# Kernel optimization log

Measured on AMD Instinct MI355X. Metric: run time of the kernel, lower is better.

The kernel has to match this reference:

```python
import jax, jax.numpy as jnp
import numpy as np

N_NODES = 100000
N_EDGES = 1600000
IN_FEATS = 128
HIDDEN = 128
OUT_DIM = 128


def setup_inputs() -> dict:
    key = jax.random.key(0)
    ks = jax.random.split(key, 8)
    x = jax.random.normal(ks[0], (N_NODES, IN_FEATS), dtype=jnp.float32)
    W1 = jax.random.normal(ks[1], (IN_FEATS, HIDDEN), dtype=jnp.float32) * (1.0 / np.sqrt(IN_FEATS))
    b1 = jnp.zeros((HIDDEN,), dtype=jnp.float32)
    W2 = jax.random.normal(ks[2], (HIDDEN, HIDDEN), dtype=jnp.float32) * (1.0 / np.sqrt(HIDDEN))
    b2 = jnp.zeros((HIDDEN,), dtype=jnp.float32)
    W3 = jax.random.normal(ks[3], (HIDDEN, OUT_DIM), dtype=jnp.float32) * (1.0 / np.sqrt(HIDDEN))
    b3 = jnp.zeros((OUT_DIM,), dtype=jnp.float32)
    edge_src = jax.random.randint(ks[4], (N_EDGES,), 0, N_NODES, dtype=jnp.int32)
    edge_dst = jax.random.randint(ks[5], (N_EDGES,), 0, N_NODES, dtype=jnp.int32)
    return {"x": x, "W1": W1, "b1": b1, "W2": W2, "b2": b2, "W3": W3, "b3": b3,
            "edge_src": edge_src, "edge_dst": edge_dst}


def _mean_agg(h, edge_src, edge_dst, inv_deg):
    # gather src features, scatter-sum to dst, divide by in-degree (mean)
    summed = jax.ops.segment_sum(h[edge_src], edge_dst, num_segments=N_NODES)
    return summed * inv_deg[:, None]


def reference(x, W1, b1, W2, b2, W3, b3, edge_src, edge_dst):
    # in-degree (clamped to 1 to avoid div-by-zero, matching mean over empty = 0)
    deg = jax.ops.segment_sum(jnp.ones((N_EDGES,), dtype=jnp.float32), edge_dst,
                              num_segments=N_NODES)
    inv_deg = 1.0 / jnp.maximum(deg, 1.0)

    # DGL GINConv (eps=0, mean): h = Linear(h + mean_neighbors(h))
    h = x
    h = (h + _mean_agg(h, edge_src, edge_dst, inv_deg)) @ W1 + b1
    h = jax.nn.relu(h)  # dropout inactive in eval mode
    h = (h + _mean_agg(h, edge_src, edge_dst, inv_deg)) @ W2 + b2
    h = jax.nn.relu(h)
    h = (h + _mean_agg(h, edge_src, edge_dst, inv_deg)) @ W3 + b3
    return h
```

## Files before the change

kernel.cpp:

```cpp
#include <hip/hip_runtime.h>
#include <hip/hip_bf16.h>
#include <stdint.h>

#if __has_builtin(__builtin_amdgcn_cvt_pk_f32_fp8) && __has_builtin(__builtin_amdgcn_cvt_pk_fp8_f32)
#define FP8_HW 1
#else
#define FP8_HW 0
#include <hip/hip_fp8.h>
#endif

#define N_NODES 100000
#define N_EDGES 1600000
#define FEAT 128

#define BKT_SHIFT 8
#define BKT_SIZE  256
#define NB_BKT    391
#define BKT_CAP   5664
#define NB_SC     800
#define EPB_SC    2000

typedef uint16_t u16;
typedef uint32_t u32;
typedef __attribute__((ext_vector_type(8))) short bf16x8;
typedef __attribute__((ext_vector_type(4))) float f32x4;
typedef __attribute__((ext_vector_type(2))) float f32x2;

__device__ __forceinline__ u16 bf16_rn(float f){
  u32 u = __float_as_uint(f);
  u += 0x7FFFu + ((u >> 16) & 1u);
  return (u16)(u >> 16);
}
__device__ __forceinline__ float bf16_lo(u32 p){ return __uint_as_float(p << 16); }
__device__ __forceinline__ float bf16_hi(u32 p){ return __uint_as_float(p & 0xFFFF0000u); }

__device__ __forceinline__ void fp8x4_to_f32(u32 w, float* o){
#if FP8_HW
  f32x2 a = __builtin_amdgcn_cvt_pk_f32_fp8(w, false);
  f32x2 b = __builtin_amdgcn_cvt_pk_f32_fp8(w, true);
  o[0] = a.x; o[1] = a.y; o[2] = b.x; o[3] = b.y;
#else
  #pragma unroll
  for (int i = 0; i < 4; ++i){
    __hip_fp8_e4m3 t; t.__x = (uint8_t)((w >> (8 * i)) & 0xFF);
    o[i] = (float)t;
  }
#endif
}
__device__ __forceinline__ u32 f32x4_to_fp8(float a, float b, float c, float d){
#if FP8_HW
  u32 r = __builtin_amdgcn_cvt_pk_fp8_f32(a, b, 0, false);
  r = __builtin_amdgcn_cvt_pk_fp8_f32(c, d, r, true);
  return r;
#else
  __hip_fp8_e4m3 qa(a), qb(b), qc(c), qd(d);
  return (u32)qa.__x | ((u32)qb.__x << 8) | ((u32)qc.__x << 16) | ((u32)qd.__x << 24);
#endif
}

__device__ __forceinline__ void acc_row(uint2 r, f32x2* acc){
#if FP8_HW
  acc[0] += __builtin_amdgcn_cvt_pk_f32_fp8(r.x, false);
  acc[1] += __builtin_amdgcn_cvt_pk_f32_fp8(r.x, true);
  acc[2] += __builtin_amdgcn_cvt_pk_f32_fp8(r.y, false);
  acc[3] += __builtin_amdgcn_cvt_pk_f32_fp8(r.y, true);
#else
  float t0[4], t1[4];
  fp8x4_to_f32(r.x, t0); fp8x4_to_f32(r.y, t1);
  acc[0].x += t0[0]; acc[0].y += t0[1]; acc[1].x += t0[2]; acc[1].y += t0[3];
  acc[2].x += t1[0]; acc[2].y += t1[1]; acc[3].x += t1[2]; acc[3].y += t1[3];
#endif
}


__global__ __launch_bounds__(512) void hist_kernel(const int* __restrict__ dst,
                                                   int* __restrict__ hcnt){
  __shared__ int h[NB_BKT];
  for (int i = threadIdx.x; i < NB_BKT; i += 512) h[i] = 0;
  __syncthreads();
  int base = blockIdx.x * EPB_SC;
  for (int e = base + threadIdx.x; e < base + EPB_SC; e += 512)
    atomicAdd(&h[dst[e] >> BKT_SHIFT], 1);
  __syncthreads();
  for (int i = threadIdx.x; i < NB_BKT; i += 512)
    hcnt[blockIdx.x * NB_BKT + i] = h[i];
}

__global__ void hscan_kernel(int* __restrict__ hcnt, int* __restrict__ cursor){
  __shared__ int s[256];
  int b = blockIdx.x, t = threadIdx.x;
  int v[4]; int sum = 0;
  #pragma unroll
  for (int j = 0; j < 4; ++j){
    int blk = 4 * t + j;
    v[j] = (blk < NB_SC) ? hcnt[blk * NB_BKT + b] : 0;
    sum += v[j];
  }
  s[t] = sum;
  __syncthreads();
  for (int d = 1; d < 256; d <<= 1){
    int add = (t >= d) ? s[t - d] : 0;
    __syncthreads();
    s[t] += add;
    __syncthreads();
  }
  int excl = s[t] - sum;
  #pragma unroll
  for (int j = 0; j < 4; ++j){
    int blk = 4 * t + j;
    if (blk < NB_SC){ hcnt[blk * NB_BKT + b] = excl; excl += v[j]; }
  }
  if (t == 255) cursor[b] = s[255];
}

__global__ __launch_bounds__(512) void scatter_kernel(const int* __restrict__ src,
                                                      const int* __restrict__ dst,
                                                      const int* __restrict__ hcnt,
                                                      uint2* __restrict__ bbuf){
  __shared__ int cur[NB_BKT];
  for (int i = threadIdx.x; i < NB_BKT; i += 512)
    cur[i] = hcnt[blockIdx.x * NB_BKT + i];
  __syncthreads();
  int base = blockIdx.x * EPB_SC;
  for (int e = base + threadIdx.x; e < base + EPB_SC; e += 512){
    int d = dst[e];
    int b = d >> BKT_SHIFT;
    int p = atomicAdd(&cur[b], 1);
    bbuf[(size_t)b * BKT_CAP + p] = make_uint2((u32)src[e], (u32)(d & (BKT_SIZE - 1)));
  }
}

__global__ __launch_bounds__(1024) void csr_build_kernel(const uint2* __restrict__ bbuf,
                                 const int* __restrict__ cursor,
                                 int* __restrict__ offs, int* __restrict__ deg,
                                 float* __restrict__ inv_deg, int* __restrict__ eidx){
  __shared__ int hist[BKT_SIZE];
  __shared__ int s[BKT_SIZE];
  __shared__ int cu[BKT_SIZE];
  int b = blockIdx.x;
  int t = threadIdx.x;
  int lo = b * BKT_CAP;
  int hi = lo + cursor[b];
  if (t < BKT_SIZE) hist[t] = 0;
  __syncthreads();
  for (int e = lo + t; e < hi; e += 1024)
    atomicAdd(&hist[bbuf[e].y], 1);
  __syncthreads();
  int v = 0, pv = 0;
  if (t < BKT_SIZE){
    v  = hist[t];
    pv = (v + 7) & ~7;
    s[t] = pv;
  }
  __syncthreads();
  for (int d = 1; d < BKT_SIZE; d <<= 1){
    int add = (t < BKT_SIZE && t >= d) ? s[t - d] : 0;
    __syncthreads();
    if (t < BKT_SIZE && t >= d) s[t] += add;
    __syncthreads();
  }
  if (t < BKT_SIZE){
    int excl = s[t] - pv;
    int node = b * BKT_SIZE + t;
    if (node < N_NODES){
      offs[node]    = lo + excl;
      deg[node]     = v;
      inv_deg[node] = 1.0f / fmaxf((float)v, 1.0f);
      for (int p = v; p < pv; ++p) eidx[lo + excl + p] = 0;
    }
    s[t]  = excl;
    cu[t] = 0;
  }
  __syncthreads();
  for (int e = lo + t; e < hi; e += 1024){
    uint2 q = bbuf[e];
    int p = atomicAdd(&cu[q.y], 1);
    eidx[lo + s[q.y] + p] = (int)q.x;
  }
}


__global__ void cvt_x8_kernel(const float* __restrict__ x, uint2* __restrict__ X8){
  int i = blockIdx.x * 256 + threadIdx.x;
  const float4* p = (const float4*)x + (size_t)i * 2;
  float4 a = p[0], b = p[1];
  uint2 o;
  o.x = f32x4_to_fp8(a.x, a.y, a.z, a.w);
  o.y = f32x4_to_fp8(b.x, b.y, b.z, b.w);
  X8[i] = o;
}

__global__ void wprep3_kernel(const float* __restrict__ W1, const float* __restrict__ W2,
                              const float* __restrict__ W3, u16* __restrict__ Wp1,
                              u16* __restrict__ Wp2, u16* __restrict__ Wp3){
  int which = blockIdx.x >> 6;
  int b     = blockIdx.x & 63;
  const float* W = (which == 0) ? W1 : (which == 1) ? W2 : W3;
  u16*        Wp = (which == 0) ? Wp1 : (which == 1) ? Wp2 : Wp3;
  int idx = b * 256 + threadIdx.x;
  int j    = idx & 7;
  int lane = (idx >> 3) & 63;
  int t    = idx >> 9;
  int k0 = t & 3, n0 = t >> 2;
  int k = k0 * 32 + (lane >> 4) * 8 + j;
  int n = n0 * 16 + (lane & 15);
  Wp[idx] = bf16_rn(W[k * FEAT + n]);
}


template<int SM, int OUT>
__global__ __launch_bounds__(128, 8) void layer_kernel(
    const u32* __restrict__ n8,
    const u16* __restrict__ hb,
    const float* __restrict__ xf,
    const int* __restrict__ offs,
    const int* __restrict__ deg,
    const float* __restrict__ inv_deg,
    const int* __restrict__ eidx,
    const u16* __restrict__ Wp,
    const float* __restrict__ bias,
    u16* __restrict__ Hout,
    u32* __restrict__ H8out,
    float* __restrict__ Fout){
  __shared__ u16 Tt[16 * FEAT];
  const int tid   = threadIdx.x;
  const int wid   = tid >> 6;
  const int lane  = tid & 63;
  const int nsub  = lane >> 4;
  const int slice = lane & 15;
  const int base  = blockIdx.x * 16;
  const u32* gbase = n8 + slice * 2;

  for (int g = 0; g < 2; ++g){
    const int rrow = wid * 8 + (g << 2) + nsub;
    const int node = base + rrow;
    const int start = offs[node];
    const int cnt   = deg[node];
    const int pcnt  = (cnt + 7) & ~7;
    const int* ep = eidx + start;

    f32x2 acc[4];
    #pragma unroll
    for (int j = 0; j < 4; ++j) acc[j] = (f32x2){0.f, 0.f};

    uint2 rc[8];
    #pragma unroll
    for (int j = 0; j < 8; ++j) rc[j] = make_uint2(0u, 0u);
    if (pcnt > 0){
      uint4 q0 = *(const uint4*)ep;
      uint4 q1 = *(const uint4*)(ep + 4);
      rc[0] = *(const uint2*)(gbase + (size_t)q0.x * 32);
      rc[1] = *(const uint2*)(gbase + (size_t)q0.y * 32);
      rc[2] = *(const uint2*)(gbase + (size_t)q0.z * 32);
      rc[3] = *(const uint2*)(gbase + (size_t)q0.w * 32);
      rc[4] = *(const uint2*)(gbase + (size_t)q1.x * 32);
      rc[5] = *(const uint2*)(gbase + (size_t)q1.y * 32);
      rc[6] = *(const uint2*)(gbase + (size_t)q1.z * 32);
      rc[7] = *(const uint2*)(gbase + (size_t)q1.w * 32);
    }
    uint4 qn1 = *(const uint4*)(ep + 8);
    uint4 qn2 = *(const uint4*)(ep + 12);

    for (int e = 0; e < pcnt; e += 8){
      uint2 rn[8];
      rn[0] = *(const uint2*)(gbase + (size_t)qn1.x * 32);
      rn[1] = *(const uint2*)(gbase + (size_t)qn1.y * 32);
      rn[2] = *(const uint2*)(gbase + (size_t)qn1.z * 32);
      rn[3] = *(const uint2*)(gbase + (size_t)qn1.w * 32);
      rn[4] = *(const uint2*)(gbase + (size_t)qn2.x * 32);
      rn[5] = *(const uint2*)(gbase + (size_t)qn2.y * 32);
      rn[6] = *(const uint2*)(gbase + (size_t)qn2.z * 32);
      rn[7] = *(const uint2*)(gbase + (size_t)qn2.w * 32);
      qn1 = *(const uint4*)(ep + e + 16);
      qn2 = *(const uint4*)(ep + e + 20);
      #pragma unroll
      for (int j = 0; j < 8; ++j) acc_row(rc[j], acc);
      #pragma unroll
      for (int j = 0; j < 8; ++j) rc[j] = rn[j];
    }

    if (pcnt > cnt){
      float f = (float)(pcnt - cnt);
      uint2 rz = *(const uint2*)gbase;
      f32x2 z[4];
      #pragma unroll
      for (int j = 0; j < 4; ++j) z[j] = (f32x2){0.f, 0.f};
      acc_row(rz, z);
      #pragma unroll
      for (int j = 0; j < 4; ++j) acc[j] -= f * z[j];
    }

    const float w = inv_deg[node];
    float self[8];
    if (SM == 1){
      const float* sp = xf + (size_t)node * FEAT + slice * 8;
      float4 a = *(const float4*)sp;
      float4 b = *(const float4*)(sp + 4);
      self[0]=a.x; self[1]=a.y; self[2]=a.z; self[3]=a.w;
      self[4]=b.x; self[5]=b.y; self[6]=b.z; self[7]=b.w;
    } else {
      const u16* sp = hb + (size_t)node * FEAT + slice * 8;
      uint4 s0 = *(const uint4*)sp;
      self[0]=bf16_lo(s0.x); self[1]=bf16_hi(s0.x); self[2]=bf16_lo(s0.y); self[3]=bf16_hi(s0.y);
      self[4]=bf16_lo(s0.z); self[5]=bf16_hi(s0.z); self[6]=bf16_lo(s0.w); self[7]=bf16_hi(s0.w);
    }
    uint4 o;
    o.x = (u32)bf16_rn(self[0] + w*acc[0].x) | ((u32)bf16_rn(self[1] + w*acc[0].y) << 16);
    o.y = (u32)bf16_rn(self[2] + w*acc[1].x) | ((u32)bf16_rn(self[3] + w*acc[1].y) << 16);
    o.z = (u32)bf16_rn(self[4] + w*acc[2].x) | ((u32)bf16_rn(self[5] + w*acc[2].y) << 16);
    o.w = (u32)bf16_rn(self[6] + w*acc[3].x) | ((u32)bf16_rn(self[7] + w*acc[3].y) << 16);
    ((uint4*)Tt)[rrow * 16 + (slice ^ (rrow & 7))] = o;
  }
  __syncthreads();

  const int quad = lane >> 4;
  const int c    = lane & 15;

  bf16x8 A[4];
  #pragma unroll
  for (int k0 = 0; k0 < 4; ++k0){
    uint4 t = ((const uint4*)Tt)[c * 16 + ((quad + k0 * 4) ^ (c & 7))];
    A[k0] = *(const bf16x8*)&t;
  }
  if (OUT == 0) __syncthreads();

  f32x4 acc2[4];
  #pragma unroll
  for (int i = 0; i < 4; ++i) acc2[i] = (f32x4){0.f, 0.f, 0.f, 0.f};
  #pragma unroll
  for (int i = 0; i < 4; ++i){
    int n0 = wid * 4 + i;
    #pragma unroll
    for (int k0 = 0; k0 < 4; ++k0){
      bf16x8 b = *(const bf16x8*)(Wp + (size_t)(((n0 << 2) | k0) * 64 + lane) * 8);
      acc2[i] = __builtin_amdgcn_mfma_f32_16x16x32_bf16(A[k0], b, acc2[i], 0, 0, 0);
    }
  }
  #pragma unroll
  for (int i = 0; i < 4; ++i){
    int n0 = wid * 4 + i;
    float bv = bias[n0 * 16 + c];
    #pragma unroll
    for (int r = 0; r < 4; ++r){
      int rr  = quad * 4 + r;
      int col = n0 * 16 + c;
      if (OUT == 1){
        Fout[(size_t)(base + rr) * FEAT + col] = acc2[i][r] + bv;
      } else {
        float v = fmaxf(acc2[i][r] + bv, 0.f);
        Tt[rr * FEAT + (col ^ ((rr & 7) << 3))] = bf16_rn(v);
      }
    }
  }

  if (OUT == 0){
    __syncthreads();
    #pragma unroll
    for (int it = 0; it < 2; ++it){
      int p  = it * 128 + tid;
      int rr = p >> 4, qq = p & 15;
      int node = base + rr;
      uint4 d = ((const uint4*)Tt)[rr * 16 + (qq ^ (rr & 7))];
      *(uint4*)(Hout + (size_t)node * FEAT + qq * 8) = d;
      uint2 o8;
      o8.x = f32x4_to_fp8(bf16_lo(d.x), bf16_hi(d.x), bf16_lo(d.y), bf16_hi(d.y));
      o8.y = f32x4_to_fp8(bf16_lo(d.z), bf16_hi(d.z), bf16_lo(d.w), bf16_hi(d.w));
      *(uint2*)(H8out + (size_t)node * 32 + qq * 2) = o8;
    }
  }
}


static inline size_t align_up(size_t x){ return (x + 255) & ~(size_t)255; }

extern "C" void kernel_launch(void* const* d_in, const int* in_sizes, int n_in,
                              void* d_out, int out_size, void* d_ws, size_t ws_size,
                              hipStream_t stream){
  const float* x  = (const float*)d_in[0];
  const float* W1 = (const float*)d_in[1];
  const float* b1 = (const float*)d_in[2];
  const float* W2 = (const float*)d_in[3];
  const float* b2 = (const float*)d_in[4];
  const float* W3 = (const float*)d_in[5];
  const float* b3 = (const float*)d_in[6];
  const int* esrc = (const int*)d_in[7];
  const int* edst = (const int*)d_in[8];

  char* w = (char*)d_ws;
  int*   deg     = (int*)w;    w += align_up((size_t)N_NODES * 4);
  int*   offs    = (int*)w;    w += align_up((size_t)N_NODES * 4);
  float* inv_deg = (float*)w;  w += align_up((size_t)N_NODES * 4);
  int*   eidx    = (int*)w;    w += align_up((size_t)NB_BKT * BKT_CAP * 4);
  u16*   Wp1     = (u16*)w;    w += align_up((size_t)16384 * 2);
  u16*   Wp2     = (u16*)w;    w += align_up((size_t)16384 * 2);
  u16*   Wp3     = (u16*)w;    w += align_up((size_t)16384 * 2);
  u16*   Hb      = (u16*)w;    w += align_up((size_t)N_NODES * FEAT * 2);
  u32*   H8b     = (u32*)w;    w += align_up((size_t)N_NODES * 32 * 4);

  uint2* bbuf   = (uint2*)Hb;
  int*   cursor = (int*)H8b;
  int*   hcnt   = (int*)((char*)H8b + align_up((size_t)NB_BKT * 4));

  u16* Ha  = (u16*)d_out;
  u32* H8a = (u32*)((char*)d_out + (size_t)N_NODES * FEAT * 2);
  u32* X8  = (u32*)((char*)d_out + (size_t)N_NODES * FEAT * 3);

  hist_kernel<<<NB_SC, 512, 0, stream>>>(edst, hcnt);
  hscan_kernel<<<NB_BKT, 256, 0, stream>>>(hcnt, cursor);
  scatter_kernel<<<NB_SC, 512, 0, stream>>>(esrc, edst, hcnt, bbuf);
  csr_build_kernel<<<NB_BKT, 1024, 0, stream>>>(bbuf, cursor, offs, deg, inv_deg, eidx);

  wprep3_kernel<<<192, 256, 0, stream>>>(W1, W2, W3, Wp1, Wp2, Wp3);
  cvt_x8_kernel<<<N_EDGES / 256, 256, 0, stream>>>(x, (uint2*)X8);

  const int LAYER_BLOCKS = N_NODES / 16;

  layer_kernel<1, 0><<<LAYER_BLOCKS, 128, 0, stream>>>(
      X8, (const u16*)nullptr, x, offs, deg, inv_deg, eidx, Wp1, b1,
      Ha, H8a, (float*)nullptr);

  layer_kernel<0, 0><<<LAYER_BLOCKS, 128, 0, stream>>>(
      H8a, Ha, (const float*)nullptr, offs, deg, inv_deg, eidx, Wp2, b2,
      Hb, H8b, (float*)nullptr);

  layer_kernel<0, 1><<<LAYER_BLOCKS, 128, 0, stream>>>(
      H8b, Hb, (const float*)nullptr, offs, deg, inv_deg, eidx, Wp3, b3,
      (u16*)nullptr, (u32*)nullptr, (float*)d_out);

  (void)in_sizes; (void)n_in; (void)out_size; (void)ws_size; (void)w;
}
```

Measured before the change: 302.4 us.

## Sort nodes by degree for balanced layer blocks, fuse prep kernels, pack bucket entries

Adds a counting sort of nodes by in-degree (descending, capped at 63) and makes the layer kernels process nodes through that permutation, so the nodes sharing a block or wave have similar degrees and less lane divergence. The x conversion, weight prep and histogram kernels are merged into one launch, and bucket entries are packed into 32 bits (24-bit src, 8-bit local dst) and staged in LDS during CSR build. Costs three extra small kernels and indirect output writes, which scatter the stores and lose output locality.

```diff
diff --git a/kernel.cpp b/kernel.cpp
--- a/kernel.cpp
+++ b/kernel.cpp
@@ -19,6 +19,10 @@
 #define BKT_CAP   5664
 #define NB_SC     800
 #define EPB_SC    2000
+
+#define PREP_CVT 6250
+#define PREP_W   192
+#define PREP_H   800
 
 typedef uint16_t u16;
 typedef uint32_t u32;
@@ -73,18 +77,50 @@
 }
 
 
-__global__ __launch_bounds__(512) void hist_kernel(const int* __restrict__ dst,
-                                                   int* __restrict__ hcnt){
+__global__ __launch_bounds__(256) void prep_kernel(
+    const float* __restrict__ x,
+    const float* __restrict__ W1, const float* __restrict__ W2,
+    const float* __restrict__ W3, const int* __restrict__ edst,
+    uint2* __restrict__ X8, u16* __restrict__ Wp1, u16* __restrict__ Wp2,
+    u16* __restrict__ Wp3, int* __restrict__ hcnt, int* __restrict__ ghist){
   __shared__ int h[NB_BKT];
-  for (int i = threadIdx.x; i < NB_BKT; i += 512) h[i] = 0;
-  __syncthreads();
-  int base = blockIdx.x * EPB_SC;
-  for (int e = base + threadIdx.x; e < base + EPB_SC; e += 512)
-    atomicAdd(&h[dst[e] >> BKT_SHIFT], 1);
-  __syncthreads();
-  for (int i = threadIdx.x; i < NB_BKT; i += 512)
-    hcnt[blockIdx.x * NB_BKT + i] = h[i];
-}
+  int blk = blockIdx.x;
+  if (blk < PREP_CVT){
+    int i = blk * 256 + threadIdx.x;
+    const float4* p = (const float4*)x + (size_t)i * 2;
+    float4 a = p[0], b = p[1];
+    uint2 o;
+    o.x = f32x4_to_fp8(a.x, a.y, a.z, a.w);
+    o.y = f32x4_to_fp8(b.x, b.y, b.z, b.w);
+    X8[i] = o;
+  } else if (blk < PREP_CVT + PREP_W){
+    int b = blk - PREP_CVT;
+    int which = b >> 6;
+    const float* W = (which == 0) ? W1 : (which == 1) ? W2 : W3;
+    u16*        Wp = (which == 0) ? Wp1 : (which == 1) ? Wp2 : Wp3;
+    int idx = (b & 63) * 256 + threadIdx.x;
+    int j    = idx & 7;
+    int lane = (idx >> 3) & 63;
+    int t    = idx >> 9;
+    int k0 = t & 3, n0 = t >> 2;
+    int k = k0 * 32 + (lane >> 4) * 8 + j;
+    int n = n0 * 16 + (lane & 15);
+    Wp[idx] = bf16_rn(W[k * FEAT + n]);
+  } else if (blk < PREP_CVT + PREP_W + PREP_H){
+    int hb = blk - (PREP_CVT + PREP_W);
+    for (int i = threadIdx.x; i < NB_BKT; i += 256) h[i] = 0;
+    __syncthreads();
+    int base = hb * EPB_SC;
+    for (int e = base + threadIdx.x; e < base + EPB_SC; e += 256)
+      atomicAdd(&h[edst[e] >> BKT_SHIFT], 1);
+    __syncthreads();
+    for (int i = threadIdx.x; i < NB_BKT; i += 256)
+      hcnt[hb * NB_BKT + i] = h[i];
+  } else {
+    if (threadIdx.x < 64) ghist[threadIdx.x] = 0;
+  }
+}
+
 
 __global__ void hscan_kernel(int* __restrict__ hcnt, int* __restrict__ cursor){
   __shared__ int s[256];
@@ -116,7 +152,7 @@
 __global__ __launch_bounds__(512) void scatter_kernel(const int* __restrict__ src,
                                                       const int* __restrict__ dst,
                                                       const int* __restrict__ hcnt,
-                                                      uint2* __restrict__ bbuf){
+                                                      u32* __restrict__ bbuf){
   __shared__ int cur[NB_BKT];
   for (int i = threadIdx.x; i < NB_BKT; i += 512)
     cur[i] = hcnt[blockIdx.x * NB_BKT + i];
@@ -126,25 +162,28 @@
     int d = dst[e];
     int b = d >> BKT_SHIFT;
     int p = atomicAdd(&cur[b], 1);
-    bbuf[(size_t)b * BKT_CAP + p] = make_uint2((u32)src[e], (u32)(d & (BKT_SIZE - 1)));
-  }
-}
-
-__global__ __launch_bounds__(1024) void csr_build_kernel(const uint2* __restrict__ bbuf,
+    bbuf[(size_t)b * BKT_CAP + p] = (u32)src[e] | ((u32)(d & (BKT_SIZE - 1)) << 24);
+  }
+}
+
+__global__ __launch_bounds__(1024) void csr_build_kernel(const u32* __restrict__ bbuf,
                                  const int* __restrict__ cursor,
                                  int* __restrict__ offs, int* __restrict__ deg,
                                  float* __restrict__ inv_deg, int* __restrict__ eidx){
+  __shared__ u32 bloc[BKT_CAP];
   __shared__ int hist[BKT_SIZE];
   __shared__ int s[BKT_SIZE];
   __shared__ int cu[BKT_SIZE];
+  __shared__ int stot;
   int b = blockIdx.x;
   int t = threadIdx.x;
   int lo = b * BKT_CAP;
-  int hi = lo + cursor[b];
+  int n  = cursor[b];
+  for (int e = t; e < n; e += 1024) bloc[e] = bbuf[lo + e];
   if (t < BKT_SIZE) hist[t] = 0;
   __syncthreads();
-  for (int e = lo + t; e < hi; e += 1024)
-    atomicAdd(&hist[bbuf[e].y], 1);
+  for (int e = t; e < n; e += 1024)
+    atomicAdd(&hist[bloc[e] >> 24], 1);
   __syncthreads();
   int v = 0, pv = 0;
   if (t < BKT_SIZE){
@@ -170,41 +209,68 @@
     }
     s[t]  = excl;
     cu[t] = 0;
-  }
-  __syncthreads();
-  for (int e = lo + t; e < hi; e += 1024){
-    uint2 q = bbuf[e];
-    int p = atomicAdd(&cu[q.y], 1);
-    eidx[lo + s[q.y] + p] = (int)q.x;
-  }
-}
-
-
-__global__ void cvt_x8_kernel(const float* __restrict__ x, uint2* __restrict__ X8){
-  int i = blockIdx.x * 256 + threadIdx.x;
-  const float4* p = (const float4*)x + (size_t)i * 2;
-  float4 a = p[0], b = p[1];
-  uint2 o;
-  o.x = f32x4_to_fp8(a.x, a.y, a.z, a.w);
-  o.y = f32x4_to_fp8(b.x, b.y, b.z, b.w);
-  X8[i] = o;
-}
-
-__global__ void wprep3_kernel(const float* __restrict__ W1, const float* __restrict__ W2,
-                              const float* __restrict__ W3, u16* __restrict__ Wp1,
-                              u16* __restrict__ Wp2, u16* __restrict__ Wp3){
-  int which = blockIdx.x >> 6;
-  int b     = blockIdx.x & 63;
-  const float* W = (which == 0) ? W1 : (which == 1) ? W2 : W3;
-  u16*        Wp = (which == 0) ? Wp1 : (which == 1) ? Wp2 : Wp3;
-  int idx = b * 256 + threadIdx.x;
-  int j    = idx & 7;
-  int lane = (idx >> 3) & 63;
-  int t    = idx >> 9;
-  int k0 = t & 3, n0 = t >> 2;
-  int k = k0 * 32 + (lane >> 4) * 8 + j;
-  int n = n0 * 16 + (lane & 15);
-  Wp[idx] = bf16_rn(W[k * FEAT + n]);
+    if (t == BKT_SIZE - 1) stot = excl + pv;
+  }
+  __syncthreads();
+  for (int e = t; e < n; e += 1024){
+    u32 q = bloc[e];
+    int y = (int)(q >> 24);
+    int p = atomicAdd(&cu[y], 1);
+    eidx[lo + s[y] + p] = (int)(q & 0xFFFFFFu);
+  }
+  int tot = stot;
+  if (t < 32 && tot + 32 <= BKT_CAP) eidx[lo + tot + t] = 0;
+}
+
+
+__global__ __launch_bounds__(256) void dhist_kernel(const int* __restrict__ deg,
+                                                    int* __restrict__ ghist){
+  __shared__ int lh[64];
+  int t = threadIdx.x;
+  if (t < 64) lh[t] = 0;
+  __syncthreads();
+  int i = blockIdx.x * 256 + t;
+  if (i < N_NODES)
+    atomicAdd(&lh[63 - min(deg[i], 63)], 1);
+  __syncthreads();
+  if (t < 64 && lh[t]) atomicAdd(&ghist[t], lh[t]);
+}
+
+__global__ __launch_bounds__(64) void dscan_kernel(const int* __restrict__ ghist,
+                                                   int* __restrict__ gcur){
+  __shared__ int s[64];
+  int t = threadIdx.x;
+  int v = ghist[t];
+  s[t] = v;
+  __syncthreads();
+  for (int d = 1; d < 64; d <<= 1){
+    int add = (t >= d) ? s[t - d] : 0;
+    __syncthreads();
+    s[t] += add;
+    __syncthreads();
+  }
+  gcur[t] = s[t] - v;
+}
+
+__global__ __launch_bounds__(256) void dperm_kernel(const int* __restrict__ deg,
+                                                    int* __restrict__ gcur,
+                                                    int* __restrict__ perm){
+  __shared__ int lh[64];
+  __shared__ int lb[64];
+  int t = threadIdx.x;
+  if (t < 64) lh[t] = 0;
+  __syncthreads();
+  int i = blockIdx.x * 256 + t;
+  bool valid = i < N_NODES;
+  int k = 0, rank = 0;
+  if (valid){
+    k = 63 - min(deg[i], 63);
+    rank = atomicAdd(&lh[k], 1);
+  }
+  __syncthreads();
+  if (t < 64 && lh[t]) lb[t] = atomicAdd(&gcur[t], lh[t]);
+  __syncthreads();
+  if (valid) perm[lb[k] + rank] = i;
 }
 
 
@@ -217,23 +283,27 @@
     const int* __restrict__ deg,
     const float* __restrict__ inv_deg,
     const int* __restrict__ eidx,
+    const int* __restrict__ perm,
     const u16* __restrict__ Wp,
     const float* __restrict__ bias,
     u16* __restrict__ Hout,
     u32* __restrict__ H8out,
     float* __restrict__ Fout){
   __shared__ u16 Tt[16 * FEAT];
+  __shared__ int nid[16];
   const int tid   = threadIdx.x;
   const int wid   = tid >> 6;
   const int lane  = tid & 63;
   const int nsub  = lane >> 4;
   const int slice = lane & 15;
-  const int base  = blockIdx.x * 16;
   const u32* gbase = n8 + slice * 2;
+
+  if (tid < 16) nid[tid] = perm[blockIdx.x * 16 + tid];
+  __syncthreads();
 
   for (int g = 0; g < 2; ++g){
     const int rrow = wid * 8 + (g << 2) + nsub;
-    const int node = base + rrow;
+    const int node = nid[rrow];
     const int start = offs[node];
     const int cnt   = deg[node];
     const int pcnt  = (cnt + 7) & ~7;
@@ -345,7 +415,7 @@
       int rr  = quad * 4 + r;
       int col = n0 * 16 + c;
       if (OUT == 1){
-        Fout[(size_t)(base + rr) * FEAT + col] = acc2[i][r] + bv;
+        Fout[(size_t)nid[rr] * FEAT + col] = acc2[i][r] + bv;
       } else {
         float v = fmaxf(acc2[i][r] + bv, 0.f);
         Tt[rr * FEAT + (col ^ ((rr & 7) << 3))] = bf16_rn(v);
@@ -359,7 +429,7 @@
     for (int it = 0; it < 2; ++it){
       int p  = it * 128 + tid;
       int rr = p >> 4, qq = p & 15;
-      int node = base + rr;
+      int node = nid[rr];
       uint4 d = ((const uint4*)Tt)[rr * 16 + (qq ^ (rr & 7))];
       *(uint4*)(Hout + (size_t)node * FEAT + qq * 8) = d;
       uint2 o8;
@@ -390,6 +460,9 @@
   int*   deg     = (int*)w;    w += align_up((size_t)N_NODES * 4);
   int*   offs    = (int*)w;    w += align_up((size_t)N_NODES * 4);
   float* inv_deg = (float*)w;  w += align_up((size_t)N_NODES * 4);
+  int*   perm    = (int*)w;    w += align_up((size_t)N_NODES * 4);
+  int*   ghist   = (int*)w;    w += align_up((size_t)64 * 4);
+  int*   gcur    = (int*)w;    w += align_up((size_t)64 * 4);
   int*   eidx    = (int*)w;    w += align_up((size_t)NB_BKT * BKT_CAP * 4);
   u16*   Wp1     = (u16*)w;    w += align_up((size_t)16384 * 2);
   u16*   Wp2     = (u16*)w;    w += align_up((size_t)16384 * 2);
@@ -397,34 +470,36 @@
   u16*   Hb      = (u16*)w;    w += align_up((size_t)N_NODES * FEAT * 2);
   u32*   H8b     = (u32*)w;    w += align_up((size_t)N_NODES * 32 * 4);
 
-  uint2* bbuf   = (uint2*)Hb;
-  int*   cursor = (int*)H8b;
-  int*   hcnt   = (int*)((char*)H8b + align_up((size_t)NB_BKT * 4));
+  u32* bbuf   = (u32*)Hb;
+  int* cursor = (int*)H8b;
+  int* hcnt   = (int*)((char*)H8b + align_up((size_t)NB_BKT * 4));
 
   u16* Ha  = (u16*)d_out;
   u32* H8a = (u32*)((char*)d_out + (size_t)N_NODES * FEAT * 2);
   u32* X8  = (u32*)((char*)d_out + (size_t)N_NODES * FEAT * 3);
 
-  hist_kernel<<<NB_SC, 512, 0, stream>>>(edst, hcnt);
+  prep_kernel<<<PREP_CVT + PREP_W + PREP_H + 1, 256, 0, stream>>>(
+      x, W1, W2, W3, edst, (uint2*)X8, Wp1, Wp2, Wp3, hcnt, ghist);
   hscan_kernel<<<NB_BKT, 256, 0, stream>>>(hcnt, cursor);
   scatter_kernel<<<NB_SC, 512, 0, stream>>>(esrc, edst, hcnt, bbuf);
   csr_build_kernel<<<NB_BKT, 1024, 0, stream>>>(bbuf, cursor, offs, deg, inv_deg, eidx);
 
-  wprep3_kernel<<<192, 256, 0, stream>>>(W1, W2, W3, Wp1, Wp2, Wp3);
-  cvt_x8_kernel<<<N_EDGES / 256, 256, 0, stream>>>(x, (uint2*)X8);
+  dhist_kernel<<<NB_BKT, 256, 0, stream>>>(deg, ghist);
+  dscan_kernel<<<1, 64, 0, stream>>>(ghist, gcur);
+  dperm_kernel<<<NB_BKT, 256, 0, stream>>>(deg, gcur, perm);
 
   const int LAYER_BLOCKS = N_NODES / 16;
 
   layer_kernel<1, 0><<<LAYER_BLOCKS, 128, 0, stream>>>(
-      X8, (const u16*)nullptr, x, offs, deg, inv_deg, eidx, Wp1, b1,
+      X8, (const u16*)nullptr, x, offs, deg, inv_deg, eidx, perm, Wp1, b1,
       Ha, H8a, (float*)nullptr);
 
   layer_kernel<0, 0><<<LAYER_BLOCKS, 128, 0, stream>>>(
-      H8a, Ha, (const float*)nullptr, offs, deg, inv_deg, eidx, Wp2, b2,
+      H8a, Ha, (const float*)nullptr, offs, deg, inv_deg, eidx, perm, Wp2, b2,
       Hb, H8b, (float*)nullptr);
 
   layer_kernel<0, 1><<<LAYER_BLOCKS, 128, 0, stream>>>(
-      H8b, Hb, (const float*)nullptr, offs, deg, inv_deg, eidx, Wp3, b3,
+      H8b, Hb, (const float*)nullptr, offs, deg, inv_deg, eidx, perm, Wp3, b3,
       (u16*)nullptr, (u32*)nullptr, (float*)d_out);
 
   (void)in_sizes; (void)n_in; (void)out_size; (void)ws_size; (void)w;
```

Measured after the change: 323.1 us. 1.07x slower.
